# Kernel optimization log

Hardware: AMD Instinct MI355X
Metric: run time of the kernel (lower is better)

## Reference

```python
import jax, jax.numpy as jnp
import numpy as np

EPS = 1e-6
SINKHORN_ITERS = 8
TEMPERATURE = 1.0
B, N, D = 4, 8192, 512
E, OUT = 8, 512
H = 1


def setup_inputs() -> dict:
    key = jax.random.key(0)
    k1, k2, k3 = jax.random.split(key, 3)
    x = jax.random.normal(k1, (B, N, D), dtype=jnp.float32)
    gate_weight = jax.random.normal(k2, (H, D, E), dtype=jnp.float32)
    experts = jax.random.normal(k3, (E, D, OUT), dtype=jnp.float32) * 0.02
    return {"x": x, "gate_weight": gate_weight, "experts": experts}


def _sinkhorn(logits):
    # logits: (b, h, n, e). log(clamp(.,eps)) then alternating row/col log-normalization.
    t = jnp.log(jnp.clip(logits, EPS)) / TEMPERATURE
    for _ in range(SINKHORN_ITERS):
        t = t - jax.nn.logsumexp(t, axis=-2, keepdims=True)  # normalize over tokens n
        t = t - jax.nn.logsumexp(t, axis=-1, keepdims=True)  # normalize over experts e
    return jnp.exp(t)


def reference(x, gate_weight, experts):
    b, n, d = x.shape
    e = experts.shape[0]
    m = n // e  # tokens per expert
    xh = x[:, None, :, :]  # b 1 n d  (single-headed -> h=1)
    gate_logits = jnp.einsum('bhnd,hde->bhne', xh, gate_weight)
    gates = _sinkhorn(gate_logits)  # b h n e
    # topk over token dim n, per expert: move n to last axis for lax.top_k
    g_t = jnp.swapaxes(gates, -1, -2)  # b h e n
    vals, idx = jax.lax.top_k(g_t, m)  # (b h e m), (b h e m)
    gate_values = jnp.transpose(vals, (2, 0, 1, 3))[..., None]  # e b h m 1
    # gather routed tokens: routed[e,b,h,m,d] = x[b,h,idx[b,h,e,m],d]
    routed = jnp.take_along_axis(xh[:, :, None, :, :], idx[..., None], axis=3)  # b h e m d
    routed = jnp.transpose(routed, (2, 0, 1, 3, 4))  # e b h m d
    expert_w = experts[:, None, :, :]  # e h i o with h=1 (rearrange 'e i o -> e 1 i o')
    outputs = jnp.einsum('ebhmi,ehio->ebhmo', routed, expert_w)  # e b h m o
    outputs = outputs * gate_values
    # scatter back (set semantics, matching einx set_at)
    bh_idx = idx.reshape(b, 1, e * m)  # b h (e m)
    bh_vals = jnp.transpose(outputs, (1, 2, 0, 3, 4)).reshape(b, 1, e * m, outputs.shape[-1])
    def scat(i1, v1):
        return jnp.zeros((n, v1.shape[-1]), dtype=v1.dtype).at[i1].set(v1)
    routed_back = jax.vmap(jax.vmap(scat))(bh_idx, bh_vals)  # b h n o
    return routed_back[:, 0]  # b n o
```

## Files before the change

### kernel.cpp

```cpp
#include <hip/hip_runtime.h>
#include <hip/hip_bf16.h>

#define BB 4
#define NN 8192
#define DD 512
#define EE 8
#define OUTD 512
#define TOPM 1024
#define EPSV 1e-6f
#define ITERS 8

using s16x8 = __attribute__((ext_vector_type(8))) short;
using f32x4 = __attribute__((ext_vector_type(4))) float;
typedef unsigned long long u64;

__device__ __forceinline__ unsigned short f2bf(float f) {
  unsigned u = __float_as_uint(f);
  return (unsigned short)((u + 0x7FFFu + ((u >> 16) & 1u)) >> 16);
}

__device__ __forceinline__ void gll16(const void* g, void* l) {
  __builtin_amdgcn_global_load_lds((const __attribute__((address_space(1))) void*)g,
                                   (__attribute__((address_space(3))) void*)l, 16, 0, 0);
}

__global__ __launch_bounds__(256) void k_gate(const float* __restrict__ x,
                                              const float* __restrict__ gw,
                                              float* __restrict__ t0,
                                              unsigned short* __restrict__ xbf,
                                              int* __restrict__ eo,
                                              int* __restrict__ counts,
                                              const float* __restrict__ W,
                                              unsigned short* __restrict__ WT) {
  const int tid = threadIdx.x;
  if (blockIdx.x >= 2048) {
    __shared__ float tl[32][33];
    const int widx = blockIdx.x - 2048;
    const int e = widx >> 8, rem = widx & 255;
    const int k0 = (rem >> 4) * 32, n0 = (rem & 15) * 32;
    const int ty = tid >> 5, tx = tid & 31;
    const float* src = W + ((long)e * DD + k0) * OUTD + n0;
#pragma unroll
    for (int j = 0; j < 4; ++j)
      tl[ty + j * 8][tx] = src[(long)(ty + j * 8) * OUTD + tx];
    __syncthreads();
    unsigned short* dst = WT + ((long)e * OUTD + n0) * DD + k0;
#pragma unroll
    for (int j = 0; j < 4; ++j)
      dst[(long)(ty + j * 8) * DD + tx] = f2bf(tl[tx][ty + j * 8]);
    return;
  }
  __shared__ float ws[16][4][8];
  if (tid < 16) eo[blockIdx.x * 16 + tid] = -1;
  if (blockIdx.x == 0 && tid >= 64 && tid < 64 + BB * EE) counts[tid - 64] = 0;
  const int lane = tid & 63;
  const int wq   = tid >> 6;
  const int k2   = wq * 128 + lane * 2;
  const float* gp = gw + (long)k2 * EE;
  const float4 g0 = *(const float4*)(gp);
  const float4 g1 = *(const float4*)(gp + 4);
  const float4 g2 = *(const float4*)(gp + 8);
  const float4 g3 = *(const float4*)(gp + 12);

  const long row0 = (long)blockIdx.x * 16;
  for (int i = 0; i < 16; ++i) {
    const long row = row0 + i;
    const float2 xv = *(const float2*)(x + row * DD + k2);
    *(unsigned*)(xbf + row * DD + k2) =
        ((unsigned)f2bf(xv.y) << 16) | (unsigned)f2bf(xv.x);

    float acc[8];
    acc[0] = xv.x * g0.x + xv.y * g2.x;
    acc[1] = xv.x * g0.y + xv.y * g2.y;
    acc[2] = xv.x * g0.z + xv.y * g2.z;
    acc[3] = xv.x * g0.w + xv.y * g2.w;
    acc[4] = xv.x * g1.x + xv.y * g3.x;
    acc[5] = xv.x * g1.y + xv.y * g3.y;
    acc[6] = xv.x * g1.z + xv.y * g3.z;
    acc[7] = xv.x * g1.w + xv.y * g3.w;
    const bool o1 = lane & 1;
    float own, oth, b0, b1, b2, b3, c0, c1, v;
    own = o1 ? acc[1] : acc[0]; oth = o1 ? acc[0] : acc[1];
    b0 = own + __shfl_xor(oth, 1);
    own = o1 ? acc[3] : acc[2]; oth = o1 ? acc[2] : acc[3];
    b1 = own + __shfl_xor(oth, 1);
    own = o1 ? acc[5] : acc[4]; oth = o1 ? acc[4] : acc[5];
    b2 = own + __shfl_xor(oth, 1);
    own = o1 ? acc[7] : acc[6]; oth = o1 ? acc[6] : acc[7];
    b3 = own + __shfl_xor(oth, 1);
    const bool o2 = lane & 2;
    own = o2 ? b1 : b0; oth = o2 ? b0 : b1;
    c0 = own + __shfl_xor(oth, 2);
    own = o2 ? b3 : b2; oth = o2 ? b2 : b3;
    c1 = own + __shfl_xor(oth, 2);
    const bool o4 = lane & 4;
    own = o4 ? c1 : c0; oth = o4 ? c0 : c1;
    v = own + __shfl_xor(oth, 4);
    v += __shfl_xor(v, 8);
    v += __shfl_xor(v, 16);
    v += __shfl_xor(v, 32);
    if (lane < 8) ws[i][wq][lane] = v;
  }
  __syncthreads();
  if (tid < 128) {
    const int row = tid >> 3, e = tid & 7;
    float s = ws[row][0][e] + ws[row][1][e] + ws[row][2][e] + ws[row][3][e];
    t0[row0 * EE + tid] = logf(fmaxf(s, EPSV));
  }
}

__global__ __attribute__((amdgpu_waves_per_eu(4, 4)))
__launch_bounds__(1024) void k_topk(const float* __restrict__ t0,
                                    float* __restrict__ R,
                                    float* __restrict__ C,
                                    int* __restrict__ expert_of) {
  __shared__ unsigned key[NN];
  __shared__ int hist[4096];
  __shared__ int bcast[2];
  __shared__ int wsum[16];
  __shared__ float ws[16][8], Csh[8], Ssh[8];
  const int b = blockIdx.x >> 3, e = blockIdx.x & 7;
  const int tid = threadIdx.x;
  const int wv = tid >> 6, ln = tid & 63;
  const float* tb = t0 + (long)b * NN * EE;

  float E[8][8], u[8], dl[8];
#pragma unroll
  for (int j = 0; j < 8; ++j) {
    const float* p = tb + (long)(j * 1024 + tid) * EE;
    float4 a = *(const float4*)p, b4 = *(const float4*)(p + 4);
    E[j][0] = expf(a.x);  E[j][1] = expf(a.y);
    E[j][2] = expf(a.z);  E[j][3] = expf(a.w);
    E[j][4] = expf(b4.x); E[j][5] = expf(b4.y);
    E[j][6] = expf(b4.z); E[j][7] = expf(b4.w);
    key[j * 1024 + tid] = __float_as_uint(p[e]);
    u[j] = 1.f;
  }
#pragma unroll
  for (int j = 0; j < 8; ++j)
#pragma unroll
    for (int e2 = 0; e2 < 8; ++e2)
      asm volatile("" : "+v"(E[j][e2]));
  for (int it = 0; it < ITERS; ++it) {
    float P[8] = {0.f,0.f,0.f,0.f,0.f,0.f,0.f,0.f};
#pragma unroll
    for (int j = 0; j < 8; ++j)
#pragma unroll
      for (int e2 = 0; e2 < 8; ++e2) P[e2] += E[j][e2] * u[j];
#pragma unroll
    for (int d = 1; d <= 4; d <<= 1) {
#pragma unroll
      for (int e2 = 0; e2 < 8; ++e2) {
        float tmp = __shfl_xor(P[e2], d);
        P[e2] += ((ln & d) == (e2 & d)) ? tmp : 0.f;
      }
    }
    float pv = P[0];
#pragma unroll
    for (int e2 = 1; e2 < 8; ++e2) pv = ((ln & 7) == e2) ? P[e2] : pv;
#pragma unroll
    for (int d = 8; d < 64; d <<= 1) pv += __shfl_xor(pv, d);
    if (ln < 8) ws[wv][ln] = pv;
    __syncthreads();
    if (tid < 64) {
      const int q = ln >> 3, e2 = ln & 7;
      float s = ws[q][e2] + ws[q + 8][e2];
#pragma unroll
      for (int d = 8; d < 64; d <<= 1) s += __shfl_xor(s, d);
      if (ln < 8) { Csh[ln] = 1.f / s; Ssh[ln] = s; }
    }
    __syncthreads();
    float vv[8];
#pragma unroll
    for (int e2 = 0; e2 < 8; ++e2) vv[e2] = Csh[e2];
#pragma unroll
    for (int j = 0; j < 8; ++j) {
      float d0 = E[j][0] * vv[0];
#pragma unroll
      for (int e2 = 1; e2 < 8; ++e2) d0 += E[j][e2] * vv[e2];
      dl[j] = d0;
      u[j] = 1.f / d0;
    }
    __syncthreads();
  }
  if (e == 0) {
#pragma unroll
    for (int j = 0; j < 8; ++j) R[(long)b * NN + j * 1024 + tid] = logf(dl[j]);
    if (tid < 8) C[b * EE + tid] = logf(Ssh[tid]);
  }

  {
    int4 z4 = make_int4(0, 0, 0, 0);
    *(int4*)&hist[tid * 4] = z4;
  }
  __syncthreads();
#pragma unroll
  for (int j = 0; j < 8; ++j) {
    const int n = j * 1024 + tid;
    float f = __uint_as_float(key[n]) - logf(dl[j]);
    unsigned uk = __float_as_uint(f);
    uk = (uk & 0x80000000u) ? ~uk : (uk | 0x80000000u);
    key[n] = uk;
    atomicAdd(&hist[uk >> 20], 1);
  }
  __syncthreads();

  unsigned prefix = 0;
  int k = TOPM;
  for (int pass = 0; pass < 3; ++pass) {
    const int4 h4 = *(const int4*)&hist[tid * 4];
    const int s3 = h4.w, s2 = h4.z + s3, s1 = h4.y + s2, s0 = h4.x + s1;
    int inc = s0;
#pragma unroll
    for (int d = 1; d < 64; d <<= 1) {
      int o = __shfl_down(inc, d);
      if (ln + d < 64) inc += o;
    }
    if (ln == 0) wsum[wv] = inc;
    __syncthreads();
    if (tid == 0) {
      int run = 0;
      for (int w2 = 15; w2 >= 0; --w2) { int t2 = wsum[w2]; wsum[w2] = run; run += t2; }
    }
    __syncthreads();
    const int above = wsum[wv] + (inc - s0);
    const int c0 = above + s0, c1 = above + s1, c2 = above + s2, c3 = above + s3;
    if (c0 >= k && c1 < k)    { bcast[0] = k - c1;    bcast[1] = tid * 4 + 0; }
    if (c1 >= k && c2 < k)    { bcast[0] = k - c2;    bcast[1] = tid * 4 + 1; }
    if (c2 >= k && c3 < k)    { bcast[0] = k - c3;    bcast[1] = tid * 4 + 2; }
    if (c3 >= k && above < k) { bcast[0] = k - above; bcast[1] = tid * 4 + 3; }
    __syncthreads();
    k = bcast[0];
    const unsigned bin = (unsigned)bcast[1];
    if (pass == 0)      prefix = bin << 20;
    else if (pass == 1) prefix |= bin << 8;
    else                prefix |= bin;
    if (pass == 2) break;
    {
      int4 z4 = make_int4(0, 0, 0, 0);
      *(int4*)&hist[tid * 4] = z4;
    }
    __syncthreads();
    if (pass == 0) {
      const unsigned pa = prefix >> 20;
      for (int n = tid; n < NN; n += 1024) {
        unsigned uk = key[n];
        if ((uk >> 20) == pa) atomicAdd(&hist[(uk >> 8) & 4095], 1);
      }
    } else {
      const unsigned pb = prefix >> 8;
      for (int n = tid; n < NN; n += 1024) {
        unsigned uk = key[n];
        if ((uk >> 8) == pb) atomicAdd(&hist[uk & 255], 1);
      }
    }
    __syncthreads();
  }
  const unsigned theta = prefix;
  const int need = k;
  const int base = tid * 8;
  int c = 0;
#pragma unroll
  for (int j = 0; j < 8; ++j) if (key[base + j] == theta) ++c;
  int inc2 = c;
#pragma unroll
  for (int d = 1; d < 64; d <<= 1) {
    int o = __shfl_up(inc2, d);
    if (ln >= d) inc2 += o;
  }
  if (ln == 63) wsum[wv] = inc2;
  __syncthreads();
  if (tid == 0) {
    int runv = 0;
    for (int i = 0; i < 16; ++i) { int t2 = wsum[i]; wsum[i] = runv; runv += t2; }
  }
  __syncthreads();
  int run = wsum[wv] + inc2 - c;
  int* eo = expert_of + b * NN;
  for (int j = 0; j < 8; ++j) {
    int n = base + j;
    unsigned uk = key[n];
    bool sel = false;
    if (uk > theta) sel = true;
    else if (uk == theta) { if (run < need) sel = true; ++run; }
    if (sel) atomicMax(&eo[n], e);
  }
}

__global__ __launch_bounds__(256) void k_post(const int* __restrict__ expert_of,
                                              const float* __restrict__ t0,
                                              const float* __restrict__ R,
                                              const float* __restrict__ C,
                                              int* __restrict__ counts,
                                              int* __restrict__ lists,
                                              float* __restrict__ gvals) {
  __shared__ int hist8[8], base8[8];
  const int tid = threadIdx.x;
  if (tid < 8) hist8[tid] = 0;
  __syncthreads();
  const long i = (long)blockIdx.x * 256 + tid;
  const int b = (int)(i >> 13);
  const int e = expert_of[i];
  int lpos = -1;
  if (e >= 0) lpos = atomicAdd(&hist8[e], 1);
  __syncthreads();
  if (tid < 8 && hist8[tid] > 0)
    base8[tid] = atomicAdd(&counts[b * EE + tid], hist8[tid]);
  __syncthreads();
  if (e >= 0) {
    const int n = (int)(i & (NN - 1));
    const int be = b * EE + e;
    const int slot = be * TOPM + base8[e] + lpos;
    lists[slot] = n;
    gvals[slot] = expf(t0[i * EE + e] - C[be] - R[i]);
  }
}

__global__ __launch_bounds__(256) void k_gemm(const unsigned short* __restrict__ xbf,
                                              const unsigned short* __restrict__ WT,
                                              const int* __restrict__ counts,
                                              const int* __restrict__ lists,
                                              const float* __restrict__ gvals,
                                              const int* __restrict__ eo,
                                              float* __restrict__ out) {
  const int tid = threadIdx.x;
  if (blockIdx.x >= 1024) {
    const int row = (blockIdx.x - 1024) * 4 + (tid >> 6);
    if (eo[row] >= 0) return;
    const int ln = tid & 63;
    float4 z = make_float4(0.f, 0.f, 0.f, 0.f);
    float4* p = (float4*)(out + (long)row * OUTD) + ln;
    p[0] = z; p[64] = z;
    return;
  }
  const int id = blockIdx.x;
  const int xq = id >> 8;
  const int be = (id >> 3) & 31;
  const int yq = id & 7;
  const int b = be >> 3, e = be & 7;
  const int cnt = counts[be];
  const int r0 = yq * 128;
  if (r0 >= cnt) return;
  const int c0 = xq * 128;

  __shared__ unsigned short As[128 * 64];
  __shared__ unsigned short Bs[128 * 64];
  __shared__ int   rowTok[128];
  __shared__ float rowG[128];

  if (tid < 128) {
    int r = r0 + tid;
    rowTok[tid] = (r < cnt) ? lists[be * TOPM + r] : -1;
    rowG[tid]   = (r < cnt) ? gvals[be * TOPM + r] : 0.f;
  }
  __syncthreads();

  const int w = tid >> 6, l = tid & 63;
  const int rbase = w * 32 + (l >> 3);
  const int sL = l & 7;
  const unsigned short* xb_b = xbf + (long)b * NN * DD;
  const unsigned short* wt_e = WT + (long)e * OUTD * DD;
  int tokc[4]; int sGa[4];
#pragma unroll
  for (int c = 0; c < 4; ++c) {
    int r = rbase + c * 8;
    int tk = rowTok[r]; if (tk < 0) tk = 0;
    tokc[c] = tk;
    sGa[c] = (sL ^ (r & 7)) * 8;
  }

  const int wr = w >> 1, wc = w & 1;
  const int fr = l & 15, fq = l >> 4;
  int aoff[4][2], boff[4][2];
#pragma unroll
  for (int m = 0; m < 4; ++m) {
#pragma unroll
    for (int kk = 0; kk < 2; ++kk) {
      int row = wr * 64 + m * 16 + fr;
      aoff[m][kk] = row * 64 + (((fq + 4 * kk) ^ (row & 7)) * 8);
      int col = wc * 64 + m * 16 + fr;
      boff[m][kk] = col * 64 + (((fq + 4 * kk) ^ (col & 7)) * 8);
    }
  }

  f32x4 acc[4][4] = {};

#define STAGE(kb) {                                                          \
    int ko = (kb) * 64;                                                      \
    _Pragma("unroll")                                                        \
    for (int c = 0; c < 4; ++c) {                                            \
      int r = rbase + c * 8;                                                 \
      gll16(xb_b + (long)tokc[c] * DD + ko + sGa[c],                         \
            As + (w * 32 + c * 8) * 64);                                     \
      gll16(wt_e + (long)(c0 + r) * DD + ko + sGa[c],                        \
            Bs + (w * 32 + c * 8) * 64);                                     \
    }                                                                        \
  }

  STAGE(0);
  for (int kb = 0; kb < 8; ++kb) {
    __syncthreads();
    s16x8 af[4][2], bf_[4][2];
#pragma unroll
    for (int m = 0; m < 4; ++m) {
      af[m][0] = *(const s16x8*)(As + aoff[m][0]);
      af[m][1] = *(const s16x8*)(As + aoff[m][1]);
      bf_[m][0] = *(const s16x8*)(Bs + boff[m][0]);
      bf_[m][1] = *(const s16x8*)(Bs + boff[m][1]);
    }
    __syncthreads();
    if (kb < 7) STAGE(kb + 1);
#pragma unroll
    for (int kk = 0; kk < 2; ++kk)
#pragma unroll
      for (int m = 0; m < 4; ++m)
#pragma unroll
        for (int n = 0; n < 4; ++n)
          acc[m][n] = __builtin_amdgcn_mfma_f32_16x16x32_bf16(af[m][kk], bf_[n][kk], acc[m][n], 0, 0, 0);
  }
#undef STAGE

#pragma unroll
  for (int m = 0; m < 4; ++m) {
    int rbase2 = wr * 64 + m * 16 + fq * 4;
    int tok[4]; float g[4];
#pragma unroll
    for (int j = 0; j < 4; ++j) { tok[j] = rowTok[rbase2 + j]; g[j] = rowG[rbase2 + j]; }
#pragma unroll
    for (int n = 0; n < 4; ++n) {
      int col = c0 + wc * 64 + n * 16 + fr;
#pragma unroll
      for (int j = 0; j < 4; ++j) {
        if (tok[j] >= 0)
          out[((long)b * NN + tok[j]) * OUTD + col] = acc[m][n][j] * g[j];
      }
    }
  }
}

extern "C" void kernel_launch(void* const* d_in, const int* in_sizes, int n_in,
                              void* d_out, int out_size, void* d_ws, size_t ws_size,
                              hipStream_t stream) {
  const float* x  = (const float*)d_in[0];
  const float* gw = (const float*)d_in[1];
  const float* ex = (const float*)d_in[2];
  float* out = (float*)d_out;

  char* wsb = (char*)d_ws;
  float*          t0     = (float*)(wsb);
  unsigned short* xbf    = (unsigned short*)(wsb + (1l << 20));
  unsigned short* WT     = (unsigned short*)(wsb + (33l << 20));
  const long base = 37l << 20;
  float*          R      = (float*)(wsb + base);
  int*            eo     = (int*)  (wsb + base + (128l << 10));
  int*            lists  = (int*)  (wsb + base + (256l << 10));
  float*          gvals  = (float*)(wsb + base + (384l << 10));
  float*          C      = (float*)(wsb + base + (512l << 10));
  int*            counts = (int*)  (wsb + base + (512l << 10) + 1024);

  k_gate<<<2048 + 2048, 256, 0, stream>>>(x, gw, t0, xbf, eo, counts, ex, WT);
  k_topk<<<BB * EE, 1024, 0, stream>>>(t0, R, C, eo);
  k_post<<<128, 256, 0, stream>>>(eo, t0, R, C, counts, lists, gvals);
  k_gemm<<<1024 + (BB * NN) / 4, 256, 0, stream>>>(xbf, WT, counts, lists, gvals, eo, out);
}
```

Measured before the change: 101.2 us.

## Move bf16 conversion of x and expert weights into the topk kernel

The bf16 conversion of x and the transpose-and-convert of the expert weights move out of the gate kernel and into extra blocks of the topk kernel. The topk stage launches only 32 heavy blocks and would otherwise leave most of the GPU idle, so this conversion work is meant to fill those idle CUs and shorten the gate kernel. The transpose tile grows to 64x64 and reuses the topk shared-memory buffer. The trade-off is that the extra blocks compete for CUs with the 32 long-running topk blocks, and x is now read a second time from memory.

```diff
diff --git a/kernel.cpp b/kernel.cpp
--- a/kernel.cpp
+++ b/kernel.cpp
@@ -27,29 +27,9 @@
 __global__ __launch_bounds__(256) void k_gate(const float* __restrict__ x,
                                               const float* __restrict__ gw,
                                               float* __restrict__ t0,
-                                              unsigned short* __restrict__ xbf,
                                               int* __restrict__ eo,
-                                              int* __restrict__ counts,
-                                              const float* __restrict__ W,
-                                              unsigned short* __restrict__ WT) {
+                                              int* __restrict__ counts) {
   const int tid = threadIdx.x;
-  if (blockIdx.x >= 2048) {
-    __shared__ float tl[32][33];
-    const int widx = blockIdx.x - 2048;
-    const int e = widx >> 8, rem = widx & 255;
-    const int k0 = (rem >> 4) * 32, n0 = (rem & 15) * 32;
-    const int ty = tid >> 5, tx = tid & 31;
-    const float* src = W + ((long)e * DD + k0) * OUTD + n0;
-#pragma unroll
-    for (int j = 0; j < 4; ++j)
-      tl[ty + j * 8][tx] = src[(long)(ty + j * 8) * OUTD + tx];
-    __syncthreads();
-    unsigned short* dst = WT + ((long)e * OUTD + n0) * DD + k0;
-#pragma unroll
-    for (int j = 0; j < 4; ++j)
-      dst[(long)(ty + j * 8) * DD + tx] = f2bf(tl[tx][ty + j * 8]);
-    return;
-  }
   __shared__ float ws[16][4][8];
   if (tid < 16) eo[blockIdx.x * 16 + tid] = -1;
   if (blockIdx.x == 0 && tid >= 64 && tid < 64 + BB * EE) counts[tid - 64] = 0;
@@ -66,9 +46,6 @@
   for (int i = 0; i < 16; ++i) {
     const long row = row0 + i;
     const float2 xv = *(const float2*)(x + row * DD + k2);
-    *(unsigned*)(xbf + row * DD + k2) =
-        ((unsigned)f2bf(xv.y) << 16) | (unsigned)f2bf(xv.x);
-
     float acc[8];
     acc[0] = xv.x * g0.x + xv.y * g2.x;
     acc[1] = xv.x * g0.y + xv.y * g2.y;
@@ -113,14 +90,50 @@
 __launch_bounds__(1024) void k_topk(const float* __restrict__ t0,
                                     float* __restrict__ R,
                                     float* __restrict__ C,
-                                    int* __restrict__ expert_of) {
+                                    int* __restrict__ expert_of,
+                                    const float* __restrict__ x,
+                                    unsigned short* __restrict__ xbf,
+                                    const float* __restrict__ W,
+                                    unsigned short* __restrict__ WT) {
   __shared__ unsigned key[NN];
   __shared__ int hist[4096];
   __shared__ int bcast[2];
   __shared__ int wsum[16];
   __shared__ float ws[16][8], Csh[8], Ssh[8];
+  const int tid = threadIdx.x;
+  if (blockIdx.x >= 32) {
+    const int bid = blockIdx.x - 32;
+    if (bid < 2048) {
+      const long row = (long)bid * 16 + (tid >> 6);
+      const int off = (tid & 63) * 8;
+      const float* xr = x + row * DD + off;
+      const float4 a = *(const float4*)(xr);
+      const float4 b4 = *(const float4*)(xr + 4);
+      s16x8 xo;
+      xo[0] = (short)f2bf(a.x);  xo[1] = (short)f2bf(a.y);
+      xo[2] = (short)f2bf(a.z);  xo[3] = (short)f2bf(a.w);
+      xo[4] = (short)f2bf(b4.x); xo[5] = (short)f2bf(b4.y);
+      xo[6] = (short)f2bf(b4.z); xo[7] = (short)f2bf(b4.w);
+      *(s16x8*)(xbf + row * DD + off) = xo;
+    } else {
+      float (*tl)[65] = (float(*)[65])key;
+      const int widx = bid - 2048;
+      const int e = widx >> 6, rem = widx & 63;
+      const int k0 = (rem >> 3) * 64, n0 = (rem & 7) * 64;
+      const int ty = tid >> 6, tx = tid & 63;
+      const float* src = W + ((long)e * DD + k0) * OUTD + n0;
+#pragma unroll
+      for (int j = 0; j < 4; ++j)
+        tl[ty + j * 16][tx] = src[(long)(ty + j * 16) * OUTD + tx];
+      __syncthreads();
+      unsigned short* dst = WT + ((long)e * OUTD + n0) * DD + k0;
+#pragma unroll
+      for (int j = 0; j < 4; ++j)
+        dst[(long)(ty + j * 16) * DD + tx] = f2bf(tl[tx][ty + j * 16]);
+    }
+    return;
+  }
   const int b = blockIdx.x >> 3, e = blockIdx.x & 7;
-  const int tid = threadIdx.x;
   const int wv = tid >> 6, ln = tid & 63;
   const float* tb = t0 + (long)b * NN * EE;
 
@@ -458,8 +471,8 @@
   float*          C      = (float*)(wsb + base + (512l << 10));
   int*            counts = (int*)  (wsb + base + (512l << 10) + 1024);
 
-  k_gate<<<2048 + 2048, 256, 0, stream>>>(x, gw, t0, xbf, eo, counts, ex, WT);
-  k_topk<<<BB * EE, 1024, 0, stream>>>(t0, R, C, eo);
+  k_gate<<<2048, 256, 0, stream>>>(x, gw, t0, eo, counts);
+  k_topk<<<32 + 2048 + 512, 1024, 0, stream>>>(t0, R, C, eo, x, xbf, ex, WT);
   k_post<<<128, 256, 0, stream>>>(eo, t0, R, C, counts, lists, gvals);
   k_gemm<<<1024 + (BB * NN) / 4, 256, 0, stream>>>(xbf, WT, counts, lists, gvals, eo, out);
 }
```

After: 105.1 us. 3.9% more time.
